# Performance work log

Measured on AMD Instinct MI355X. Metric: run time of the kernel, lower is better.

Reference implementation:

```python
import jax, jax.numpy as jnp
import numpy as np

EPS = 1e-4      # scn.BatchNormLeakyReLU default eps
LEAK = 0.333    # scn default leakiness

B, P, H, Wd = 4, 1, 640, 1024
N_PER = 100_000
CIN = COUT = 128
K = 9  # 1x3x3 stencil


def _build_rulebook(rng):
    # Sample unique active voxels per event, then hash-join neighbors (vectorized).
    coords = []
    for b in range(B):
        flat = rng.choice(P * H * Wd, size=N_PER, replace=False)
        p = flat // (H * Wd)
        r = flat % (H * Wd)
        coords.append(np.stack([np.full(N_PER, b), p, r // Wd, r % Wd], axis=1))
    coords = np.concatenate(coords).astype(np.int64)  # [N,4] = (b,p,y,x)
    N = coords.shape[0]
    # flat key with +1 padding in y,x so offsets never alias across borders
    keys = ((coords[:, 0] * P + coords[:, 1]) * (H + 2) + (coords[:, 2] + 1)) * (Wd + 2) + (coords[:, 3] + 1)
    order = np.argsort(keys)
    sk = keys[order]
    offsets = [(dy, dx) for dy in (-1, 0, 1) for dx in (-1, 0, 1)]
    neigh = np.full((N, K), N, dtype=np.int32)  # sentinel N -> zero row
    for k, (dy, dx) in enumerate(offsets):
        qk = keys + dy * (Wd + 2) + dx
        pos = np.searchsorted(sk, qk)
        posc = np.clip(pos, 0, N - 1)
        found = sk[posc] == qk
        neigh[:, k] = np.where(found, order[posc].astype(np.int32), np.int32(N))
    return neigh


def setup_inputs() -> dict:
    rng = np.random.default_rng(0)
    neigh_idx = jnp.asarray(_build_rulebook(rng))  # [N,9] int32
    key = jax.random.key(0)
    k1, k2, k3 = jax.random.split(key, 3)
    N = B * N_PER
    feats = jax.random.normal(k1, (N, CIN), dtype=jnp.float32)
    W = jax.random.normal(k2, (K, CIN, COUT), dtype=jnp.float32) * 0.05
    bias = jax.random.normal(k3, (COUT,), dtype=jnp.float32) * 0.01
    gamma = jnp.ones((COUT,), dtype=jnp.float32)
    beta = jnp.zeros((COUT,), dtype=jnp.float32)
    return {"feats": feats, "W": W, "bias": bias, "gamma": gamma, "beta": beta,
            "neigh_idx": neigh_idx}


def reference(feats, W, bias, gamma, beta, neigh_idx):
    # Submanifold sparse conv: gather active neighbors per kernel tap, GEMM, accumulate.
    N = feats.shape[0]
    fp = jnp.concatenate([feats, jnp.zeros((1, feats.shape[1]), feats.dtype)], axis=0)  # zero row for missing neighbors
    out = jnp.broadcast_to(bias, (N, W.shape[2])).astype(feats.dtype)
    for k in range(K):  # fixed small loop over kernel taps
        out = out + fp[neigh_idx[:, k]] @ W[k]  # [N,Cin] @ [Cin,Cout]
    # BatchNorm (training stats over active sites) + LeakyReLU, fused
    mean = out.mean(axis=0)
    var = out.var(axis=0)
    y = (out - mean) * jax.lax.rsqrt(var + EPS) * gamma + beta
    return jnp.where(y > 0, y, LEAK * y)
```

## Files before the change

kernel.cpp:

```cpp
#include <hip/hip_runtime.h>
#include <hip/hip_bf16.h>
#include <stdint.h>

#define N_PTS 400000
#define K_TAPS 9
#define CIN 128
#define COUT 128
#define EPS_BN 1e-4f
#define LEAK 0.333f

typedef __bf16 bf16x8 __attribute__((ext_vector_type(8)));
typedef float floatx16 __attribute__((ext_vector_type(16)));

#define PACKW_BYTES (K_TAPS * 8 * 4 * 64 * 8 * 2)
#define SUMS_OFF PACKW_BYTES
#define SUMSQ_OFF (SUMS_OFF + 512)
#define AB_OFF (SUMSQ_OFF + 512)
#define FEATSB_OFF (AB_OFF + 1024)
#define PREBN_OFF (FEATSB_OFF + (size_t)(N_PTS + 1) * CIN * 2)
#define WS_NEED_A (PREBN_OFF + (size_t)N_PTS * COUT * 2)

__device__ inline unsigned int pack_bf16_rn(float lo, float hi) {
    unsigned int a = __float_as_uint(lo) + 0x8000u;
    unsigned int b = __float_as_uint(hi) + 0x8000u;
    return (a >> 16) | (b & 0xffff0000u);
}

__device__ inline void gload_lds16(const void* g, void* l) {
    __builtin_amdgcn_global_load_lds(
        (const __attribute__((address_space(1))) unsigned int*)g,
        (__attribute__((address_space(3))) unsigned int*)l, 16, 0, 0);
}

__global__ __launch_bounds__(256) void convert_feats_kernel(
    const float* __restrict__ f, __hip_bfloat16* __restrict__ o) {
    if (blockIdx.x == 25000) {
        if (threadIdx.x < 16) {
            uint4 z = {0u, 0u, 0u, 0u};
            *(uint4*)(o + (size_t)N_PTS * CIN + threadIdx.x * 8) = z;
        }
        return;
    }
    size_t i = ((size_t)blockIdx.x * 256 + threadIdx.x) * 8;
    const float4* f4 = (const float4*)(f + i);
    float4 a = f4[0], b = f4[1];
    uint4 v;
    v.x = pack_bf16_rn(a.x, a.y);
    v.y = pack_bf16_rn(a.z, a.w);
    v.z = pack_bf16_rn(b.x, b.y);
    v.w = pack_bf16_rn(b.z, b.w);
    *(uint4*)(o + i) = v;
}

__global__ void pack_w_kernel(const float* __restrict__ W,
                              __hip_bfloat16* __restrict__ pw,
                              float* __restrict__ gsum) {
    if (blockIdx.x == 288) {
        ((float4*)gsum)[threadIdx.x] = make_float4(0.f, 0.f, 0.f, 0.f);
        return;
    }
    int frag = blockIdx.x;
    int lane = threadIdx.x;
    int t = frag & 3;
    int c = (frag >> 2) & 7;
    int k = frag >> 5;
    int n = lane & 31;
    int kk0 = (lane >> 5) * 8;
    const float* src = W + (size_t)k * CIN * COUT + (size_t)(c * 16 + kk0) * COUT + (t * 32 + n);
    __hip_bfloat16* dst = pw + (size_t)frag * 512 + lane * 8;
#pragma unroll
    for (int j = 0; j < 8; ++j) dst[j] = (__hip_bfloat16)src[(size_t)j * COUT];
}

__device__ inline void stage_tap(char* smem, const char* pwb, int k, int buf,
                                 int wave, int lane) {
    const char* g = pwb + (size_t)k * 32768;
    char* l = smem + buf * 32768;
#pragma unroll
    for (int i = 0; i < 4; ++i) {
        int chunk = i * 8 + wave;
        gload_lds16(g + (size_t)chunk * 1024 + (size_t)lane * 16, l + (size_t)chunk * 1024);
    }
}

template <bool GATHER_BF16, bool OUT_BF16>
__global__ __launch_bounds__(512, 4) void spconv_gemm_kernel(
    const void* __restrict__ feats_any,
    const __hip_bfloat16* __restrict__ packw,
    const int* __restrict__ neigh,
    void* __restrict__ out_any,
    float* __restrict__ gsum, float* __restrict__ gsumsq) {
    __shared__ __align__(16) char smem[65536];

    const int tid = threadIdx.x;
    const int wave = tid >> 6;
    const int lane = tid & 63;
    const int hj = lane >> 5;
    const int m = lane & 31;
    const int row = blockIdx.x * 256 + wave * 32 + m;
    const bool rvalid = (row < N_PTS);
    const size_t nbase = (size_t)row * K_TAPS;

    floatx16 acc[4];
#pragma unroll
    for (int t = 0; t < 4; ++t)
#pragma unroll
        for (int r = 0; r < 16; ++r) acc[t][r] = 0.0f;

    const char* pwb = (const char*)packw;

    if constexpr (GATHER_BF16) {
        const __hip_bfloat16* fb = (const __hip_bfloat16*)feats_any;
        uint4 av[8];
        int nbA, nbB;

        nbA = rvalid ? neigh[nbase + 0] : N_PTS;
        nbB = rvalid ? neigh[nbase + 1] : N_PTS;
        stage_tap(smem, pwb, 0, 0, wave, lane);
        __builtin_amdgcn_sched_barrier(0);
        {
            const uint4* ar = (const uint4*)(fb + (size_t)nbA * CIN);
#pragma unroll
            for (int c = 0; c < 8; ++c) av[c] = ar[c * 2 + hj];
        }
        __builtin_amdgcn_sched_barrier(0);
        asm volatile("s_waitcnt vmcnt(8)" ::: "memory");
        __builtin_amdgcn_s_barrier();

#pragma unroll
        for (int k = 0; k < K_TAPS; ++k) {
            const int cur = k & 1;
            if (k + 2 < K_TAPS) {
                int v = rvalid ? neigh[nbase + k + 2] : N_PTS;
                if (cur == 0) nbA = v; else nbB = v;
            }
            if (k + 1 < K_TAPS) stage_tap(smem, pwb, k + 1, cur ^ 1, wave, lane);
            __builtin_amdgcn_sched_barrier(0);

            const char* bbase = smem + (size_t)cur * 32768;
            const int nbn = (cur == 0) ? nbB : nbA;
            const uint4* arn = (const uint4*)(fb + (size_t)nbn * CIN);

            __builtin_amdgcn_s_setprio(1);
#pragma unroll
            for (int c = 0; c < 8; ++c) {
                bf16x8 afrag = __builtin_bit_cast(bf16x8, av[c]);
#pragma unroll
                for (int t = 0; t < 4; ++t) {
                    bf16x8 bfrag = __builtin_bit_cast(
                        bf16x8, *(const uint4*)(bbase + (c * 4 + t) * 1024 + lane * 16));
                    acc[t] = __builtin_amdgcn_mfma_f32_32x32x16_bf16(afrag, bfrag, acc[t], 0, 0, 0);
                }
                if (k + 1 < K_TAPS) av[c] = arn[c * 2 + hj];
            }
            __builtin_amdgcn_s_setprio(0);
            __builtin_amdgcn_sched_barrier(0);

            if (k + 1 < K_TAPS) {
                asm volatile("s_waitcnt vmcnt(8)" ::: "memory");
                __builtin_amdgcn_s_barrier();
            }
        }
    } else {
        int nb[K_TAPS];
#pragma unroll
        for (int k = 0; k < K_TAPS; ++k)
            nb[k] = rvalid ? neigh[nbase + k] : N_PTS;
        stage_tap(smem, pwb, 0, 0, wave, lane);
        __syncthreads();
#pragma unroll
        for (int k = 0; k < K_TAPS; ++k) {
            const int cur = k & 1;
            const bool valid = (nb[k] < N_PTS);
            const int safe = valid ? nb[k] : 0;
            uint4 a8[8];
            const float4* ar = (const float4*)((const float*)feats_any + (size_t)safe * CIN);
#pragma unroll
            for (int c = 0; c < 8; ++c) {
                float4 f0 = ar[c * 4 + hj * 2];
                float4 f1 = ar[c * 4 + hj * 2 + 1];
                a8[c].x = pack_bf16_rn(f0.x, f0.y);
                a8[c].y = pack_bf16_rn(f0.z, f0.w);
                a8[c].z = pack_bf16_rn(f1.x, f1.y);
                a8[c].w = pack_bf16_rn(f1.z, f1.w);
            }
            if (k + 1 < K_TAPS) stage_tap(smem, pwb, k + 1, cur ^ 1, wave, lane);
            if (!valid) {
#pragma unroll
                for (int c = 0; c < 8; ++c) { a8[c].x = 0u; a8[c].y = 0u; a8[c].z = 0u; a8[c].w = 0u; }
            }
            const char* bbase = smem + (size_t)cur * 32768;
#pragma unroll
            for (int c = 0; c < 8; ++c) {
                bf16x8 afrag = __builtin_bit_cast(bf16x8, a8[c]);
#pragma unroll
                for (int t = 0; t < 4; ++t) {
                    bf16x8 bfrag = __builtin_bit_cast(
                        bf16x8, *(const uint4*)(bbase + (c * 4 + t) * 1024 + lane * 16));
                    acc[t] = __builtin_amdgcn_mfma_f32_32x32x16_bf16(afrag, bfrag, acc[t], 0, 0, 0);
                }
            }
            __syncthreads();
        }
    }

    __syncthreads();

#pragma unroll
    for (int t = 0; t < 4; ++t) {
#pragma unroll
        for (int r = 0; r < 16; ++r) {
            int row_local = (r & 3) + 8 * (r >> 2) + 4 * hj;
            size_t grow = (size_t)blockIdx.x * 256 + wave * 32 + row_local;
            if (grow < N_PTS) {
                if (OUT_BF16)
                    ((__hip_bfloat16*)out_any)[grow * COUT + (t * 32 + m)] =
                        (__hip_bfloat16)acc[t][r];
                else
                    ((float*)out_any)[grow * COUT + (t * 32 + m)] = acc[t][r];
            }
        }
    }

    float s[4], q[4];
#pragma unroll
    for (int t = 0; t < 4; ++t) {
        s[t] = 0.0f; q[t] = 0.0f;
#pragma unroll
        for (int r = 0; r < 16; ++r) {
            float v = acc[t][r];
            s[t] += v;
            q[t] += v * v;
        }
        s[t] += __shfl_xor(s[t], 32, 64);
        q[t] += __shfl_xor(q[t], 32, 64);
    }

    float* lsum = (float*)smem;
    float* lsq = (float*)(smem + 4096);
    if (hj == 0) {
#pragma unroll
        for (int t = 0; t < 4; ++t) {
            lsum[wave * 128 + t * 32 + m] = s[t];
            lsq[wave * 128 + t * 32 + m] = q[t];
        }
    }
    __syncthreads();
    if (tid < 128) {
        float ts = 0.0f, tq = 0.0f;
#pragma unroll
        for (int w = 0; w < 8; ++w) {
            ts += lsum[w * 128 + tid];
            tq += lsq[w * 128 + tid];
        }
        atomicAdd(&gsum[tid], ts);
        atomicAdd(&gsumsq[tid], tq);
    }
}

__global__ __launch_bounds__(256) void bn_lrelu_bf16_kernel(
    const __hip_bfloat16* __restrict__ pre, float* __restrict__ out,
    const float* __restrict__ gsum, const float* __restrict__ gsumsq,
    const float* __restrict__ gamma, const float* __restrict__ beta) {
    __shared__ float ab[256];
    const int tid = threadIdx.x;
    if (tid < 128) {
        const float inv_n = 1.0f / (float)N_PTS;
        float mean = gsum[tid] * inv_n;
        float var = gsumsq[tid] * inv_n - mean * mean;
        float a = gamma[tid] * rsqrtf(var + EPS_BN);
        ab[tid] = a;
        ab[128 + tid] = beta[tid] - mean * a;
    }
    __syncthreads();

    size_t i = ((size_t)blockIdx.x * 256 + tid) * 4;
    int c = (int)(i & (COUT - 1));
    uint2 v = *(const uint2*)(pre + i);
    float x0 = __uint_as_float((v.x & 0xffffu) << 16);
    float x1 = __uint_as_float((v.x >> 16) << 16);
    float x2 = __uint_as_float((v.y & 0xffffu) << 16);
    float x3 = __uint_as_float((v.y >> 16) << 16);
    float y0 = fmaf(ab[c], x0, ab[128 + c]);
    float y1 = fmaf(ab[c + 1], x1, ab[128 + c + 1]);
    float y2 = fmaf(ab[c + 2], x2, ab[128 + c + 2]);
    float y3 = fmaf(ab[c + 3], x3, ab[128 + c + 3]);
    float4 o;
    o.x = (y0 > 0.0f) ? y0 : LEAK * y0;
    o.y = (y1 > 0.0f) ? y1 : LEAK * y1;
    o.z = (y2 > 0.0f) ? y2 : LEAK * y2;
    o.w = (y3 > 0.0f) ? y3 : LEAK * y3;
    *(float4*)(out + i) = o;
}

__global__ __launch_bounds__(256) void bn_lrelu_f32_kernel(
    float* __restrict__ out,
    const float* __restrict__ gsum, const float* __restrict__ gsumsq,
    const float* __restrict__ gamma, const float* __restrict__ beta) {
    __shared__ float ab[256];
    const int tid = threadIdx.x;
    if (tid < 128) {
        const float inv_n = 1.0f / (float)N_PTS;
        float mean = gsum[tid] * inv_n;
        float var = gsumsq[tid] * inv_n - mean * mean;
        float a = gamma[tid] * rsqrtf(var + EPS_BN);
        ab[tid] = a;
        ab[128 + tid] = beta[tid] - mean * a;
    }
    __syncthreads();

    size_t i = ((size_t)blockIdx.x * 256 + tid) * 4;
    int c = (int)(i & (COUT - 1));
    float4 v = *(const float4*)(out + i);
    v.x = fmaf(ab[c], v.x, ab[128 + c]);
    v.y = fmaf(ab[c + 1], v.y, ab[128 + c + 1]);
    v.z = fmaf(ab[c + 2], v.z, ab[128 + c + 2]);
    v.w = fmaf(ab[c + 3], v.w, ab[128 + c + 3]);
    v.x = (v.x > 0.0f) ? v.x : LEAK * v.x;
    v.y = (v.y > 0.0f) ? v.y : LEAK * v.y;
    v.z = (v.z > 0.0f) ? v.z : LEAK * v.z;
    v.w = (v.w > 0.0f) ? v.w : LEAK * v.w;
    *(float4*)(out + i) = v;
}

extern "C" void kernel_launch(void* const* d_in, const int* in_sizes, int n_in,
                              void* d_out, int out_size, void* d_ws, size_t ws_size,
                              hipStream_t stream) {
    const float* feats = (const float*)d_in[0];
    const float* W = (const float*)d_in[1];
    const float* gamma = (const float*)d_in[3];
    const float* beta = (const float*)d_in[4];
    const int* neigh = (const int*)d_in[5];
    float* out = (float*)d_out;

    char* ws = (char*)d_ws;
    __hip_bfloat16* packw = (__hip_bfloat16*)ws;
    float* gsum = (float*)(ws + SUMS_OFF);
    float* gsumsq = (float*)(ws + SUMSQ_OFF);

    const int gemm_grid = (N_PTS + 255) / 256;

    hipLaunchKernelGGL(pack_w_kernel, dim3(289), dim3(64), 0, stream, W, packw, gsum);

    if (ws_size >= WS_NEED_A) {
        __hip_bfloat16* featsb = (__hip_bfloat16*)(ws + FEATSB_OFF);
        __hip_bfloat16* prebn = (__hip_bfloat16*)(ws + PREBN_OFF);
        hipLaunchKernelGGL(convert_feats_kernel, dim3(25001), dim3(256), 0, stream, feats, featsb);
        hipLaunchKernelGGL((spconv_gemm_kernel<true, true>), dim3(gemm_grid), dim3(512), 0,
                           stream, (const void*)featsb, packw, neigh, (void*)prebn, gsum, gsumsq);
        hipLaunchKernelGGL(bn_lrelu_bf16_kernel, dim3(50000), dim3(256), 0, stream,
                           prebn, out, gsum, gsumsq, gamma, beta);
    } else {
        hipLaunchKernelGGL((spconv_gemm_kernel<false, false>), dim3(gemm_grid), dim3(512), 0,
                           stream, (const void*)feats, packw, neigh, (void*)out, gsum, gsumsq);
        hipLaunchKernelGGL(bn_lrelu_f32_kernel, dim3(100000), dim3(256), 0, stream,
                           out, gsum, gsumsq, gamma, beta);
    }
}
```

Measured before the change: 527.8 us.

## Give each wave two 32-row M tiles to reuse LDS weight fragments

Each block still covers 256 rows, but now uses 4 waves of 256 threads instead of 8, and each wave computes two 32-row M tiles. Every B fragment read from LDS is therefore reused across two MFMA row tiles, which halves LDS reads per MFMA. Weight staging is spread over 4 waves, and the gather prefetch and vmcnt waits are widened to match. The cost is double the accumulator and prefetch registers (launch bounds 256,2), lower occupancy, and fewer waves to hide gather latency.

```diff
diff --git a/kernel.cpp b/kernel.cpp
--- a/kernel.cpp
+++ b/kernel.cpp
@@ -77,14 +77,14 @@
     const char* g = pwb + (size_t)k * 32768;
     char* l = smem + buf * 32768;
 #pragma unroll
-    for (int i = 0; i < 4; ++i) {
-        int chunk = i * 8 + wave;
+    for (int i = 0; i < 8; ++i) {
+        int chunk = i * 4 + wave;
         gload_lds16(g + (size_t)chunk * 1024 + (size_t)lane * 16, l + (size_t)chunk * 1024);
     }
 }
 
 template <bool GATHER_BF16, bool OUT_BF16>
-__global__ __launch_bounds__(512, 4) void spconv_gemm_kernel(
+__global__ __launch_bounds__(256, 2) void spconv_gemm_kernel(
     const void* __restrict__ feats_any,
     const __hip_bfloat16* __restrict__ packw,
     const int* __restrict__ neigh,
@@ -97,107 +97,131 @@
     const int lane = tid & 63;
     const int hj = lane >> 5;
     const int m = lane & 31;
-    const int row = blockIdx.x * 256 + wave * 32 + m;
-    const bool rvalid = (row < N_PTS);
-    const size_t nbase = (size_t)row * K_TAPS;
-
-    floatx16 acc[4];
-#pragma unroll
-    for (int t = 0; t < 4; ++t)
-#pragma unroll
-        for (int r = 0; r < 16; ++r) acc[t][r] = 0.0f;
+    const int row0 = blockIdx.x * 256 + wave * 64 + m;
+    const int row1 = row0 + 32;
+    const bool rv0 = (row0 < N_PTS);
+    const bool rv1 = (row1 < N_PTS);
+    const size_t nbase0 = (size_t)row0 * K_TAPS;
+    const size_t nbase1 = (size_t)row1 * K_TAPS;
+
+    floatx16 acc[2][4];
+#pragma unroll
+    for (int mt = 0; mt < 2; ++mt)
+#pragma unroll
+        for (int t = 0; t < 4; ++t)
+#pragma unroll
+            for (int r = 0; r < 16; ++r) acc[mt][t][r] = 0.0f;
 
     const char* pwb = (const char*)packw;
 
     if constexpr (GATHER_BF16) {
         const __hip_bfloat16* fb = (const __hip_bfloat16*)feats_any;
-        uint4 av[8];
-        int nbA, nbB;
-
-        nbA = rvalid ? neigh[nbase + 0] : N_PTS;
-        nbB = rvalid ? neigh[nbase + 1] : N_PTS;
+        uint4 av[2][8];
+        int nA0, nA1, nB0, nB1;
+
+        nA0 = rv0 ? neigh[nbase0 + 0] : N_PTS;
+        nA1 = rv1 ? neigh[nbase1 + 0] : N_PTS;
+        nB0 = rv0 ? neigh[nbase0 + 1] : N_PTS;
+        nB1 = rv1 ? neigh[nbase1 + 1] : N_PTS;
         stage_tap(smem, pwb, 0, 0, wave, lane);
         __builtin_amdgcn_sched_barrier(0);
         {
-            const uint4* ar = (const uint4*)(fb + (size_t)nbA * CIN);
-#pragma unroll
-            for (int c = 0; c < 8; ++c) av[c] = ar[c * 2 + hj];
+            const uint4* a0 = (const uint4*)(fb + (size_t)nA0 * CIN);
+            const uint4* a1 = (const uint4*)(fb + (size_t)nA1 * CIN);
+#pragma unroll
+            for (int c = 0; c < 8; ++c) {
+                av[0][c] = a0[c * 2 + hj];
+                av[1][c] = a1[c * 2 + hj];
+            }
         }
         __builtin_amdgcn_sched_barrier(0);
-        asm volatile("s_waitcnt vmcnt(8)" ::: "memory");
+        asm volatile("s_waitcnt vmcnt(16)" ::: "memory");
         __builtin_amdgcn_s_barrier();
 
 #pragma unroll
         for (int k = 0; k < K_TAPS; ++k) {
             const int cur = k & 1;
             if (k + 2 < K_TAPS) {
-                int v = rvalid ? neigh[nbase + k + 2] : N_PTS;
-                if (cur == 0) nbA = v; else nbB = v;
+                int v0 = rv0 ? neigh[nbase0 + k + 2] : N_PTS;
+                int v1 = rv1 ? neigh[nbase1 + k + 2] : N_PTS;
+                if (cur == 0) { nA0 = v0; nA1 = v1; } else { nB0 = v0; nB1 = v1; }
             }
             if (k + 1 < K_TAPS) stage_tap(smem, pwb, k + 1, cur ^ 1, wave, lane);
             __builtin_amdgcn_sched_barrier(0);
 
             const char* bbase = smem + (size_t)cur * 32768;
-            const int nbn = (cur == 0) ? nbB : nbA;
-            const uint4* arn = (const uint4*)(fb + (size_t)nbn * CIN);
+            const int nbn0 = (cur == 0) ? nB0 : nA0;
+            const int nbn1 = (cur == 0) ? nB1 : nA1;
+            const uint4* an0 = (const uint4*)(fb + (size_t)nbn0 * CIN);
+            const uint4* an1 = (const uint4*)(fb + (size_t)nbn1 * CIN);
 
             __builtin_amdgcn_s_setprio(1);
 #pragma unroll
             for (int c = 0; c < 8; ++c) {
-                bf16x8 afrag = __builtin_bit_cast(bf16x8, av[c]);
-#pragma unroll
-                for (int t = 0; t < 4; ++t) {
-                    bf16x8 bfrag = __builtin_bit_cast(
+                bf16x8 bfrag[4];
+#pragma unroll
+                for (int t = 0; t < 4; ++t)
+                    bfrag[t] = __builtin_bit_cast(
                         bf16x8, *(const uint4*)(bbase + (c * 4 + t) * 1024 + lane * 16));
-                    acc[t] = __builtin_amdgcn_mfma_f32_32x32x16_bf16(afrag, bfrag, acc[t], 0, 0, 0);
+#pragma unroll
+                for (int mt = 0; mt < 2; ++mt) {
+                    bf16x8 afrag = __builtin_bit_cast(bf16x8, av[mt][c]);
+#pragma unroll
+                    for (int t = 0; t < 4; ++t)
+                        acc[mt][t] = __builtin_amdgcn_mfma_f32_32x32x16_bf16(
+                            afrag, bfrag[t], acc[mt][t], 0, 0, 0);
                 }
-                if (k + 1 < K_TAPS) av[c] = arn[c * 2 + hj];
+                if (k + 1 < K_TAPS) {
+                    av[0][c] = an0[c * 2 + hj];
+                    av[1][c] = an1[c * 2 + hj];
+                }
             }
             __builtin_amdgcn_s_setprio(0);
             __builtin_amdgcn_sched_barrier(0);
 
             if (k + 1 < K_TAPS) {
-                asm volatile("s_waitcnt vmcnt(8)" ::: "memory");
+                asm volatile("s_waitcnt vmcnt(16)" ::: "memory");
                 __builtin_amdgcn_s_barrier();
             }
         }
     } else {
-        int nb[K_TAPS];
-#pragma unroll
-        for (int k = 0; k < K_TAPS; ++k)
-            nb[k] = rvalid ? neigh[nbase + k] : N_PTS;
+        int nb0[K_TAPS], nb1[K_TAPS];
+#pragma unroll
+        for (int k = 0; k < K_TAPS; ++k) {
+            nb0[k] = rv0 ? neigh[nbase0 + k] : N_PTS;
+            nb1[k] = rv1 ? neigh[nbase1 + k] : N_PTS;
+        }
         stage_tap(smem, pwb, 0, 0, wave, lane);
         __syncthreads();
 #pragma unroll
         for (int k = 0; k < K_TAPS; ++k) {
             const int cur = k & 1;
-            const bool valid = (nb[k] < N_PTS);
-            const int safe = valid ? nb[k] : 0;
-            uint4 a8[8];
-            const float4* ar = (const float4*)((const float*)feats_any + (size_t)safe * CIN);
-#pragma unroll
-            for (int c = 0; c < 8; ++c) {
-                float4 f0 = ar[c * 4 + hj * 2];
-                float4 f1 = ar[c * 4 + hj * 2 + 1];
-                a8[c].x = pack_bf16_rn(f0.x, f0.y);
-                a8[c].y = pack_bf16_rn(f0.z, f0.w);
-                a8[c].z = pack_bf16_rn(f1.x, f1.y);
-                a8[c].w = pack_bf16_rn(f1.z, f1.w);
-            }
             if (k + 1 < K_TAPS) stage_tap(smem, pwb, k + 1, cur ^ 1, wave, lane);
-            if (!valid) {
-#pragma unroll
-                for (int c = 0; c < 8; ++c) { a8[c].x = 0u; a8[c].y = 0u; a8[c].z = 0u; a8[c].w = 0u; }
-            }
             const char* bbase = smem + (size_t)cur * 32768;
 #pragma unroll
-            for (int c = 0; c < 8; ++c) {
-                bf16x8 afrag = __builtin_bit_cast(bf16x8, a8[c]);
-#pragma unroll
-                for (int t = 0; t < 4; ++t) {
-                    bf16x8 bfrag = __builtin_bit_cast(
-                        bf16x8, *(const uint4*)(bbase + (c * 4 + t) * 1024 + lane * 16));
-                    acc[t] = __builtin_amdgcn_mfma_f32_32x32x16_bf16(afrag, bfrag, acc[t], 0, 0, 0);
+            for (int mt = 0; mt < 2; ++mt) {
+                const int nb = (mt == 0) ? nb0[k] : nb1[k];
+                const bool valid = (nb < N_PTS);
+                const int safe = valid ? nb : 0;
+                const float4* ar = (const float4*)((const float*)feats_any + (size_t)safe * CIN);
+#pragma unroll
+                for (int c = 0; c < 8; ++c) {
+                    float4 f0 = ar[c * 4 + hj * 2];
+                    float4 f1 = ar[c * 4 + hj * 2 + 1];
+                    uint4 a;
+                    a.x = pack_bf16_rn(f0.x, f0.y);
+                    a.y = pack_bf16_rn(f0.z, f0.w);
+                    a.z = pack_bf16_rn(f1.x, f1.y);
+                    a.w = pack_bf16_rn(f1.z, f1.w);
+                    if (!valid) { a.x = 0u; a.y = 0u; a.z = 0u; a.w = 0u; }
+                    bf16x8 afrag = __builtin_bit_cast(bf16x8, a);
+#pragma unroll
+                    for (int t = 0; t < 4; ++t) {
+                        bf16x8 bfrag = __builtin_bit_cast(
+                            bf16x8, *(const uint4*)(bbase + (c * 4 + t) * 1024 + lane * 16));
+                        acc[mt][t] = __builtin_amdgcn_mfma_f32_32x32x16_bf16(
+                            afrag, bfrag, acc[mt][t], 0, 0, 0);
+                    }
                 }
             }
             __syncthreads();
@@ -207,17 +231,20 @@
     __syncthreads();
 
 #pragma unroll
-    for (int t = 0; t < 4; ++t) {
-#pragma unroll
-        for (int r = 0; r < 16; ++r) {
-            int row_local = (r & 3) + 8 * (r >> 2) + 4 * hj;
-            size_t grow = (size_t)blockIdx.x * 256 + wave * 32 + row_local;
-            if (grow < N_PTS) {
-                if (OUT_BF16)
-                    ((__hip_bfloat16*)out_any)[grow * COUT + (t * 32 + m)] =
-                        (__hip_bfloat16)acc[t][r];
-                else
-                    ((float*)out_any)[grow * COUT + (t * 32 + m)] = acc[t][r];
+    for (int mt = 0; mt < 2; ++mt) {
+#pragma unroll
+        for (int t = 0; t < 4; ++t) {
+#pragma unroll
+            for (int r = 0; r < 16; ++r) {
+                int row_local = (r & 3) + 8 * (r >> 2) + 4 * hj;
+                size_t grow = (size_t)blockIdx.x * 256 + wave * 64 + mt * 32 + row_local;
+                if (grow < N_PTS) {
+                    if (OUT_BF16)
+                        ((__hip_bfloat16*)out_any)[grow * COUT + (t * 32 + m)] =
+                            (__hip_bfloat16)acc[mt][t][r];
+                    else
+                        ((float*)out_any)[grow * COUT + (t * 32 + m)] = acc[mt][t][r];
+                }
             }
         }
     }
@@ -227,17 +254,19 @@
     for (int t = 0; t < 4; ++t) {
         s[t] = 0.0f; q[t] = 0.0f;
 #pragma unroll
-        for (int r = 0; r < 16; ++r) {
-            float v = acc[t][r];
-            s[t] += v;
-            q[t] += v * v;
-        }
+        for (int mt = 0; mt < 2; ++mt)
+#pragma unroll
+            for (int r = 0; r < 16; ++r) {
+                float v = acc[mt][t][r];
+                s[t] += v;
+                q[t] += v * v;
+            }
         s[t] += __shfl_xor(s[t], 32, 64);
         q[t] += __shfl_xor(q[t], 32, 64);
     }
 
     float* lsum = (float*)smem;
-    float* lsq = (float*)(smem + 4096);
+    float* lsq = (float*)(smem + 2048);
     if (hj == 0) {
 #pragma unroll
         for (int t = 0; t < 4; ++t) {
@@ -249,7 +278,7 @@
     if (tid < 128) {
         float ts = 0.0f, tq = 0.0f;
 #pragma unroll
-        for (int w = 0; w < 8; ++w) {
+        for (int w = 0; w < 4; ++w) {
             ts += lsum[w * 128 + tid];
             tq += lsq[w * 128 + tid];
         }
@@ -346,12 +375,12 @@
         __hip_bfloat16* featsb = (__hip_bfloat16*)(ws + FEATSB_OFF);
         __hip_bfloat16* prebn = (__hip_bfloat16*)(ws + PREBN_OFF);
         hipLaunchKernelGGL(convert_feats_kernel, dim3(25001), dim3(256), 0, stream, feats, featsb);
-        hipLaunchKernelGGL((spconv_gemm_kernel<true, true>), dim3(gemm_grid), dim3(512), 0,
+        hipLaunchKernelGGL((spconv_gemm_kernel<true, true>), dim3(gemm_grid), dim3(256), 0,
                            stream, (const void*)featsb, packw, neigh, (void*)prebn, gsum, gsumsq);
         hipLaunchKernelGGL(bn_lrelu_bf16_kernel, dim3(50000), dim3(256), 0, stream,
                            prebn, out, gsum, gsumsq, gamma, beta);
     } else {
-        hipLaunchKernelGGL((spconv_gemm_kernel<false, false>), dim3(gemm_grid), dim3(512), 0,
+        hipLaunchKernelGGL((spconv_gemm_kernel<false, false>), dim3(gemm_grid), dim3(256), 0,
                            stream, (const void*)feats, packw, neigh, (void*)out, gsum, gsumsq);
         hipLaunchKernelGGL(bn_lrelu_f32_kernel, dim3(100000), dim3(256), 0, stream,
                            out, gsum, gsumsq, gamma, beta);
```

New measurement: 546.9 us. +3.6%, slower.
